# Optimization experiments

Measured on AMD Instinct MI355X. Metric: run time of the kernel, lower is better.

Reference implementation:

```python
import jax, jax.numpy as jnp
import numpy as np

N, D = 8192, 1024

def setup_inputs() -> dict:
    key = jax.random.key(0)
    ks = jax.random.split(key, 7)
    s = 1.0 / np.sqrt(D)
    return {
        "sent_mat": jax.random.normal(ks[0], (N, D), dtype=jnp.float32),
        "indicator": 0,
        "Wq": jax.random.normal(ks[1], (D, D), dtype=jnp.float32) * s,
        "bq": jax.random.normal(ks[2], (D,), dtype=jnp.float32) * s,
        "Wk": jax.random.normal(ks[3], (D, D), dtype=jnp.float32) * s,
        "bk": jax.random.normal(ks[4], (D,), dtype=jnp.float32) * s,
        "Wv": jax.random.normal(ks[5], (D, D), dtype=jnp.float32) * s,
        "bv": jax.random.normal(ks[6], (D,), dtype=jnp.float32) * s,
    }

def reference(sent_mat, indicator, Wq, bq, Wk, bk, Wv, bv):
    # torch.nn.Linear: y = x @ W.T + b
    Q = sent_mat @ Wq.T + bq            # [N, D]
    K = sent_mat @ Wk.T + bk            # [N, D]
    V = sent_mat @ Wv.T + bv            # [N, D]
    sim = Q @ K.T                       # [N, N]
    if indicator == 0:                  # custom score inversion
        sim = 1.0 - sim
    sim_norm = sim / jnp.sqrt(jnp.asarray(D, dtype=sim.dtype))
    # NOTE: softmax over dim=0 (columns normalized over rows), unconventional
    attn_w = jax.nn.softmax(sim_norm, axis=0)   # [N, N]
    attn_out = attn_w @ V               # [N, D]
    return (attn_out, attn_w)
```

## Files before the change

kernel.cpp:

```cpp
#include <hip/hip_runtime.h>

#define NT 8192
#define DM 1024

typedef unsigned short u16;
typedef __bf16 bf16x8 __attribute__((ext_vector_type(8)));
typedef float f32x4 __attribute__((ext_vector_type(4)));
typedef u16 u16x8 __attribute__((ext_vector_type(8)));

__device__ __forceinline__ u16 f2bf(float f) {
  union { float f; unsigned u; } v; v.f = f;
  unsigned r = v.u + 0x7fffu + ((v.u >> 16) & 1u);
  return (u16)(r >> 16);
}
__device__ __forceinline__ float bf2f(u16 h) {
  union { unsigned u; float f; } v; v.u = ((unsigned)h) << 16;
  return v.f;
}

__device__ __forceinline__ void stage16(const u16* g, u16* lds_wave_uniform) {
  __builtin_amdgcn_global_load_lds(
      (const __attribute__((address_space(1))) unsigned int*)g,
      (__attribute__((address_space(3))) unsigned int*)lds_wave_uniform, 16, 0, 0);
}

__global__ void cvt_bf16_kernel(const float* __restrict__ in, u16* __restrict__ out, int n4) {
  int i = blockIdx.x * blockDim.x + threadIdx.x;
  int stride = gridDim.x * blockDim.x;
  for (; i < n4; i += stride) {
    float4 v = reinterpret_cast<const float4*>(in)[i];
    ushort4 o;
    o.x = f2bf(v.x); o.y = f2bf(v.y); o.z = f2bf(v.z); o.w = f2bf(v.w);
    reinterpret_cast<ushort4*>(out)[i] = o;
  }
}

__global__ __launch_bounds__(512, 2)
void qkt_exp_256(const u16* __restrict__ Q, const u16* __restrict__ Kmat, int K,
                 u16* __restrict__ E, float* __restrict__ cs,
                 const int* __restrict__ indp) {
  __shared__ u16 AT[2][256 * 64];
  __shared__ u16 BT[2][256 * 64];
  const int t = threadIdx.x;
  const int l = t & 63;
  const int w = t >> 6;
  const int wm = w >> 2;
  const int wn = w & 3;
  const int r16 = l & 15;
  const int half = l >> 4;

  const int gx = gridDim.x;
  const int nwg = gx * gridDim.y;
  int lin = blockIdx.y * gx + blockIdx.x;
  if ((nwg & 7) == 0) lin = (lin & 7) * (nwg >> 3) + (lin >> 3);
  const int bx = lin % gx;
  const int by = lin / gx;
  const size_t brow = (size_t)by * 256;
  const size_t bcol = (size_t)bx * 256;

  const int srow = w * 8 + (l >> 3);
  const int kel = ((l & 7) ^ (l >> 3)) * 8;
  const int ntiles = K >> 6;

  f32x4 acc[8][4] = {};

#pragma unroll
  for (int q = 0; q < 4; ++q) {
    stage16(Q    + (brow + q * 64 + srow) * (size_t)K + kel, &AT[0][q * 4096 + w * 512]);
    stage16(Kmat + (bcol + q * 64 + srow) * (size_t)K + kel, &BT[0][q * 4096 + w * 512]);
  }
  __syncthreads();

  for (int tt = 0; tt < ntiles; ++tt) {
    const int cur = tt & 1;
    const int nxt = cur ^ 1;
    const int k1 = (tt + 1) << 6;
    const bool more = (tt + 1 < ntiles);
#pragma unroll
    for (int p = 0; p < 4; ++p) {
      if (p == 0 && more) {
#pragma unroll
        for (int q = 0; q < 4; ++q)
          stage16(Q + (brow + q * 64 + srow) * (size_t)K + (k1 + kel),
                  &AT[nxt][q * 4096 + w * 512]);
      }
      if (p == 1 && more) {
#pragma unroll
        for (int q = 0; q < 4; ++q)
          stage16(Kmat + (bcol + q * 64 + srow) * (size_t)K + (k1 + kel),
                  &BT[nxt][q * 4096 + w * 512]);
      }
      bf16x8 af[4][2], bfr[2][2];
#pragma unroll
      for (int m = 0; m < 4; ++m) {
        const int row = wm * 128 + (p >> 1) * 64 + m * 16 + r16;
#pragma unroll
        for (int kk = 0; kk < 2; ++kk) {
          const int slot = (half + 4 * kk) ^ (r16 & 7);
          af[m][kk] = *reinterpret_cast<const bf16x8*>(&AT[cur][row * 64 + slot * 8]);
        }
      }
#pragma unroll
      for (int n = 0; n < 2; ++n) {
        const int row = wn * 64 + (p & 1) * 32 + n * 16 + r16;
#pragma unroll
        for (int kk = 0; kk < 2; ++kk) {
          const int slot = (half + 4 * kk) ^ (r16 & 7);
          bfr[n][kk] = *reinterpret_cast<const bf16x8*>(&BT[cur][row * 64 + slot * 8]);
        }
      }
      __builtin_amdgcn_s_setprio(1);
#pragma unroll
      for (int m = 0; m < 4; ++m)
#pragma unroll
        for (int n = 0; n < 2; ++n)
#pragma unroll
          for (int kk = 0; kk < 2; ++kk)
            acc[(p >> 1) * 4 + m][(p & 1) * 2 + n] = __builtin_amdgcn_mfma_f32_16x16x32_bf16(
                af[m][kk], bfr[n][kk], acc[(p >> 1) * 4 + m][(p & 1) * 2 + n], 0, 0, 0);
      __builtin_amdgcn_s_setprio(0);
      __builtin_amdgcn_sched_barrier(0);
    }
    __syncthreads();
  }

  const bool flip = (*indp == 0);
  const float cexp = 0.045084220027780106f;
  float csum[4] = {0.f, 0.f, 0.f, 0.f};
#pragma unroll
  for (int mg = 0; mg < 8; ++mg) {
#pragma unroll
    for (int ng = 0; ng < 4; ++ng) {
#pragma unroll
      for (int q = 0; q < 4; ++q) {
        float s = acc[mg][ng][q];
        float x = flip ? (1.0f - s) : s;
        float e = exp2f(x * cexp);
        size_t row = brow + wm * 128 + mg * 16 + half * 4 + q;
        size_t col = bcol + wn * 64 + ng * 16 + r16;
        E[row * NT + col] = f2bf(e);
        csum[ng] += e;
      }
    }
  }
#pragma unroll
  for (int ng = 0; ng < 4; ++ng) {
    float s = csum[ng];
    s += __shfl_xor(s, 16);
    s += __shfl_xor(s, 32);
    if (l < 16) atomicAdd(&cs[bcol + wn * 64 + ng * 16 + l], s);
  }
}

template<int EPI>
__global__ __launch_bounds__(512, 2)
void mega_bt(const u16* __restrict__ A, const u16* __restrict__ B, int K, int ldo,
             const float* __restrict__ bias, u16* __restrict__ obf,
             float* __restrict__ of32, float* __restrict__ cs,
             const int* __restrict__ indp) {
  __shared__ u16 AT[3][256 * 64];
  __shared__ u16 BT[3][128 * 64];
  const int t = threadIdx.x;
  const int l = t & 63;
  const int w = t >> 6;
  const int wm = w >> 2;
  const int wn = w & 3;
  const int r16 = l & 15;
  const int half = l >> 4;

  const int gx = gridDim.x;
  const int nwg = gx * gridDim.y;
  int lin = blockIdx.y * gx + blockIdx.x;
  if ((nwg & 7) == 0) lin = (lin & 7) * (nwg >> 3) + (lin >> 3);
  const int bx = lin % gx;
  const int by = lin / gx;
  const size_t brow = (size_t)by * 256;
  const size_t bcol = (size_t)bx * 128;

  const int srow = w * 8 + (l >> 3);
  const int kel = ((l & 7) ^ (l >> 3)) * 8;
  const int nt = K >> 6;

  f32x4 acc[8][2] = {};

#define STAGE(tile, buf)                                                              \
  {                                                                                   \
    const int k0_ = (tile) << 6;                                                      \
    _Pragma("unroll")                                                                 \
    for (int q = 0; q < 4; ++q)                                                       \
      stage16(A + (brow + q * 64 + srow) * (size_t)K + (k0_ + kel),                   \
              &AT[buf][q * 4096 + w * 512]);                                          \
    _Pragma("unroll")                                                                 \
    for (int q = 0; q < 2; ++q)                                                       \
      stage16(B + (bcol + q * 64 + srow) * (size_t)K + (k0_ + kel),                   \
              &BT[buf][q * 4096 + w * 512]);                                          \
  }

  STAGE(0, 0);
  STAGE(1, 1);

  for (int tt = 0; tt < nt; ++tt) {
    const int cur = tt % 3;
    if (tt < nt - 1) asm volatile("s_waitcnt vmcnt(6)" ::: "memory");
    else             asm volatile("s_waitcnt vmcnt(0)" ::: "memory");
    __builtin_amdgcn_s_barrier();
    __builtin_amdgcn_sched_barrier(0);
    if (tt + 2 < nt) STAGE(tt + 2, (tt + 2) % 3);
    __builtin_amdgcn_sched_barrier(0);

    bf16x8 bfr[2][2];
#pragma unroll
    for (int n = 0; n < 2; ++n) {
      const int row = wn * 32 + n * 16 + r16;
#pragma unroll
      for (int kk = 0; kk < 2; ++kk) {
        const int slot = (half + 4 * kk) ^ (r16 & 7);
        bfr[n][kk] = *reinterpret_cast<const bf16x8*>(&BT[cur][row * 64 + slot * 8]);
      }
    }
#pragma unroll
    for (int p = 0; p < 2; ++p) {
      bf16x8 af[4][2];
#pragma unroll
      for (int m = 0; m < 4; ++m) {
        const int row = wm * 128 + p * 64 + m * 16 + r16;
#pragma unroll
        for (int kk = 0; kk < 2; ++kk) {
          const int slot = (half + 4 * kk) ^ (r16 & 7);
          af[m][kk] = *reinterpret_cast<const bf16x8*>(&AT[cur][row * 64 + slot * 8]);
        }
      }
      __builtin_amdgcn_s_setprio(1);
#pragma unroll
      for (int m = 0; m < 4; ++m)
#pragma unroll
        for (int n = 0; n < 2; ++n)
#pragma unroll
          for (int kk = 0; kk < 2; ++kk)
            acc[p * 4 + m][n] = __builtin_amdgcn_mfma_f32_16x16x32_bf16(
                af[m][kk], bfr[n][kk], acc[p * 4 + m][n], 0, 0, 0);
      __builtin_amdgcn_s_setprio(0);
      __builtin_amdgcn_sched_barrier(0);
    }
  }
#undef STAGE

  if constexpr (EPI == 0) {
#pragma unroll
    for (int mg = 0; mg < 8; ++mg) {
#pragma unroll
      for (int n = 0; n < 2; ++n) {
        const int cc = wn * 32 + n * 16 + r16;
        const float bv = bias[bcol + cc];
#pragma unroll
        for (int q = 0; q < 4; ++q) {
          size_t row = brow + wm * 128 + mg * 16 + half * 4 + q;
          obf[row * (size_t)ldo + bcol + cc] = f2bf(acc[mg][n][q] + bv);
        }
      }
    }
  } else if constexpr (EPI == 1) {
    const bool flip = (*indp == 0);
    const float cexp = 0.045084220027780106f;
    float csum[2] = {0.f, 0.f};
#pragma unroll
    for (int mg = 0; mg < 8; ++mg) {
#pragma unroll
      for (int n = 0; n < 2; ++n) {
        const int cc = wn * 32 + n * 16 + r16;
#pragma unroll
        for (int q = 0; q < 4; ++q) {
          float s = acc[mg][n][q];
          float x = flip ? (1.0f - s) : s;
          float e = exp2f(x * cexp);
          size_t row = brow + wm * 128 + mg * 16 + half * 4 + q;
          obf[row * (size_t)ldo + bcol + cc] = f2bf(e);
          csum[n] += e;
        }
      }
    }
#pragma unroll
    for (int n = 0; n < 2; ++n) {
      float s = csum[n];
      s += __shfl_xor(s, 16);
      s += __shfl_xor(s, 32);
      if (l < 16) atomicAdd(&cs[bcol + wn * 32 + n * 16 + l], s);
    }
  } else {
#pragma unroll
    for (int mg = 0; mg < 8; ++mg) {
#pragma unroll
      for (int n = 0; n < 2; ++n) {
#pragma unroll
        for (int q = 0; q < 4; ++q) {
          size_t row = brow + wm * 128 + mg * 16 + half * 4 + q;
          size_t col = bcol + wn * 32 + n * 16 + r16;
          of32[row * (size_t)ldo + col] = acc[mg][n][q];
        }
      }
    }
  }
}

template<int EPI, int AF32, int BF32>
__global__ __launch_bounds__(256)
void gemm_bt(const void* __restrict__ Av, const void* __restrict__ Bv, int K, int ldo,
             const float* __restrict__ bias, u16* __restrict__ obf,
             float* __restrict__ of32, const int* __restrict__ indp) {
  __shared__ u16 As[128 * 32];
  __shared__ u16 Bs[128 * 32];
  const int t = threadIdx.x;
  const int l = t & 63;
  const int w = t >> 6;
  const int wr = w >> 1;
  const int wc = w & 1;
  const int r16 = l & 15;
  const int half = l >> 4;

  const int gx = gridDim.x;
  const int nwg = gx * gridDim.y;
  int lin = blockIdx.y * gx + blockIdx.x;
  if ((nwg & 7) == 0) lin = (lin & 7) * (nwg >> 3) + (lin >> 3);
  const int bx = lin % gx;
  const int by = lin / gx;

  const size_t brow = (size_t)by * 128;
  const size_t bcol = (size_t)bx * 128;
  const int kel = (l & 3) * 8;
  const int lrow = l >> 2;

  f32x4 acc[4][4] = {};

  for (int k0 = 0; k0 < K; k0 += 32) {
#pragma unroll
    for (int c = 0; c < 2; ++c) {
      const int seg = c * 4 + w;
      const int r = seg * 16 + lrow;
      if constexpr (AF32) {
        const float* ga = (const float*)Av + (brow + r) * (size_t)K + (k0 + kel);
        float4 u0 = *reinterpret_cast<const float4*>(ga);
        float4 u1 = *reinterpret_cast<const float4*>(ga + 4);
        u16x8 o;
        o[0] = f2bf(u0.x); o[1] = f2bf(u0.y); o[2] = f2bf(u0.z); o[3] = f2bf(u0.w);
        o[4] = f2bf(u1.x); o[5] = f2bf(u1.y); o[6] = f2bf(u1.z); o[7] = f2bf(u1.w);
        *reinterpret_cast<u16x8*>(&As[seg * 512 + l * 8]) = o;
      } else {
        const u16* ga = (const u16*)Av + (brow + r) * (size_t)K + (k0 + kel);
        stage16(ga, &As[seg * 512]);
      }
      if constexpr (BF32) {
        const float* gb = (const float*)Bv + (bcol + r) * (size_t)K + (k0 + kel);
        float4 u0 = *reinterpret_cast<const float4*>(gb);
        float4 u1 = *reinterpret_cast<const float4*>(gb + 4);
        u16x8 o;
        o[0] = f2bf(u0.x); o[1] = f2bf(u0.y); o[2] = f2bf(u0.z); o[3] = f2bf(u0.w);
        o[4] = f2bf(u1.x); o[5] = f2bf(u1.y); o[6] = f2bf(u1.z); o[7] = f2bf(u1.w);
        *reinterpret_cast<u16x8*>(&Bs[seg * 512 + l * 8]) = o;
      } else {
        const u16* gb = (const u16*)Bv + (bcol + r) * (size_t)K + (k0 + kel);
        stage16(gb, &Bs[seg * 512]);
      }
    }
    __syncthreads();
    bf16x8 af[4], bfv[4];
#pragma unroll
    for (int m = 0; m < 4; ++m)
      af[m] = *reinterpret_cast<const bf16x8*>(&As[(wr * 64 + m * 16 + r16) * 32 + half * 8]);
#pragma unroll
    for (int n = 0; n < 4; ++n)
      bfv[n] = *reinterpret_cast<const bf16x8*>(&Bs[(wc * 64 + n * 16 + r16) * 32 + half * 8]);
#pragma unroll
    for (int m = 0; m < 4; ++m)
#pragma unroll
      for (int n = 0; n < 4; ++n)
        acc[m][n] = __builtin_amdgcn_mfma_f32_16x16x32_bf16(af[m], bfv[n], acc[m][n], 0, 0, 0);
    __syncthreads();
  }

  const int crow0 = wr * 64 + half * 4;
  const int ccol0 = wc * 64 + r16;

  if constexpr (EPI == 0) {
#pragma unroll
    for (int m = 0; m < 4; ++m) {
#pragma unroll
      for (int n = 0; n < 4; ++n) {
        const int cc = ccol0 + n * 16;
        const float bv = bias[bcol + cc];
#pragma unroll
        for (int q = 0; q < 4; ++q) {
          size_t idx = (brow + crow0 + m * 16 + q) * (size_t)ldo + (bcol + cc);
          obf[idx] = f2bf(acc[m][n][q] + bv);
        }
      }
    }
  } else if constexpr (EPI == 1) {
    const bool flip = (*indp == 0);
    const float cexp = 0.045084220027780106f;
#pragma unroll
    for (int m = 0; m < 4; ++m) {
#pragma unroll
      for (int n = 0; n < 4; ++n) {
        const int cc = ccol0 + n * 16;
#pragma unroll
        for (int q = 0; q < 4; ++q) {
          float s = acc[m][n][q];
          float x = flip ? (1.0f - s) : s;
          size_t idx = (brow + crow0 + m * 16 + q) * (size_t)ldo + (bcol + cc);
          of32[idx] = exp2f(x * cexp);
        }
      }
    }
  } else {
#pragma unroll
    for (int m = 0; m < 4; ++m) {
#pragma unroll
      for (int n = 0; n < 4; ++n) {
        const int cc = ccol0 + n * 16;
#pragma unroll
        for (int q = 0; q < 4; ++q) {
          size_t idx = (brow + crow0 + m * 16 + q) * (size_t)ldo + (bcol + cc);
          of32[idx] = acc[m][n][q];
        }
      }
    }
  }
}

__global__ void colsum_kernel(const float* __restrict__ E, float* __restrict__ cs) {
  const int col = blockIdx.x * 256 + threadIdx.x;
  const int r0 = blockIdx.y * 256;
  float s = 0.f;
  for (int r = r0; r < r0 + 256; ++r)
    s += E[(size_t)r * NT + col];
  atomicAdd(&cs[col], s);
}

__global__ void norm_kernel(float* __restrict__ w, const float* __restrict__ cs, int n4) {
  int i = blockIdx.x * blockDim.x + threadIdx.x;
  int stride = gridDim.x * blockDim.x;
  for (; i < n4; i += stride) {
    float4 v = reinterpret_cast<float4*>(w)[i];
    int j4 = i & (NT / 4 - 1);
    float4 c = reinterpret_cast<const float4*>(cs)[j4];
    v.x /= c.x; v.y /= c.y; v.z /= c.z; v.w /= c.w;
    reinterpret_cast<float4*>(w)[i] = v;
  }
}

__global__ void norm_bf16_kernel(const u16* __restrict__ e, float* __restrict__ w,
                                 const float* __restrict__ cs, int n4) {
  int i = blockIdx.x * blockDim.x + threadIdx.x;
  int stride = gridDim.x * blockDim.x;
  for (; i < n4; i += stride) {
    ushort4 ev = reinterpret_cast<const ushort4*>(e)[i];
    int j4 = i & (NT / 4 - 1);
    float4 c = reinterpret_cast<const float4*>(cs)[j4];
    float4 v;
    v.x = bf2f(ev.x) / c.x;
    v.y = bf2f(ev.y) / c.y;
    v.z = bf2f(ev.z) / c.z;
    v.w = bf2f(ev.w) / c.w;
    reinterpret_cast<float4*>(w)[i] = v;
  }
}

__global__ void vt_kernel(const u16* __restrict__ Vb, const float* __restrict__ cs,
                          u16* __restrict__ Vt) {
  __shared__ u16 tile[64][65];
  const int jb = blockIdx.x * 64;
  const int db = blockIdx.y * 64;
  const int t = threadIdx.x;
  {
    const int d = t & 63;
    const int j0 = t >> 6;
    for (int jj = j0; jj < 64; jj += 4)
      tile[jj][d] = Vb[(size_t)(jb + jj) * DM + db + d];
  }
  __syncthreads();
  {
    const int j = t & 63;
    const int d0 = t >> 6;
    const float inv = cs ? (1.0f / cs[jb + j]) : 1.0f;
    for (int dd = d0; dd < 64; dd += 4) {
      u16 raw = tile[j][dd];
      Vt[(size_t)(db + dd) * NT + jb + j] = cs ? f2bf(bf2f(raw) * inv) : raw;
    }
  }
}

extern "C" void kernel_launch(void* const* d_in, const int* in_sizes, int n_in,
                              void* d_out, int out_size, void* d_ws, size_t ws_size,
                              hipStream_t stream) {
  const float* X  = (const float*)d_in[0];
  const int* indp = (const int*)d_in[1];
  const float* Wq = (const float*)d_in[2];
  const float* bq = (const float*)d_in[3];
  const float* Wk = (const float*)d_in[4];
  const float* bk = (const float*)d_in[5];
  const float* Wv = (const float*)d_in[6];
  const float* bv = (const float*)d_in[7];

  float* attn_out = (float*)d_out;
  float* attn_w   = (float*)d_out + (size_t)NT * DM;

  const size_t EB_BYTES = (size_t)NT * NT * 2;
  const size_t QKV_BYTES = (size_t)NT * DM * 2;
  const size_t need_fast = EB_BYTES + 4 * QKV_BYTES + NT * 4;

  if (ws_size >= need_fast) {
    char* ws = (char*)d_ws;
    u16* Eb = (u16*)ws;
    u16* Qb = (u16*)(ws + EB_BYTES);
    u16* Kb = Qb + (size_t)NT * DM;
    u16* Vb = Kb + (size_t)NT * DM;
    u16* Vt = Vb + (size_t)NT * DM;
    float* cs = (float*)(Vt + (size_t)NT * DM);
    u16* Xb  = Eb;
    u16* Wqb = Eb + (size_t)NT * DM;
    u16* Wkb = Wqb + (size_t)DM * DM;
    u16* Wvb = Wkb + (size_t)DM * DM;

    cvt_bf16_kernel<<<2048, 256, 0, stream>>>(X,  Xb,  NT * DM / 4);
    cvt_bf16_kernel<<<1024, 256, 0, stream>>>(Wq, Wqb, DM * DM / 4);
    cvt_bf16_kernel<<<1024, 256, 0, stream>>>(Wk, Wkb, DM * DM / 4);
    cvt_bf16_kernel<<<1024, 256, 0, stream>>>(Wv, Wvb, DM * DM / 4);

    dim3 gqkv(DM / 128, NT / 256);
    mega_bt<0><<<gqkv, 512, 0, stream>>>(Xb, Wqb, DM, DM, bq, Qb, nullptr, nullptr, nullptr);
    mega_bt<0><<<gqkv, 512, 0, stream>>>(Xb, Wkb, DM, DM, bk, Kb, nullptr, nullptr, nullptr);
    mega_bt<0><<<gqkv, 512, 0, stream>>>(Xb, Wvb, DM, DM, bv, Vb, nullptr, nullptr, nullptr);

    hipMemsetAsync(cs, 0, NT * sizeof(float), stream);
    qkt_exp_256<<<dim3(NT / 256, NT / 256), 512, 0, stream>>>(Qb, Kb, DM, Eb, cs, indp);

    vt_kernel<<<dim3(NT / 64, DM / 64), 256, 0, stream>>>(Vb, cs, Vt);

    mega_bt<2><<<dim3(DM / 128, NT / 256), 512, 0, stream>>>(
        Eb, Vt, NT, DM, nullptr, nullptr, attn_out, nullptr, nullptr);

    norm_bf16_kernel<<<4096, 256, 0, stream>>>(Eb, attn_w, cs, NT * NT / 4);
  } else {
    char* ws = (char*)d_ws;
    u16* Qb = (u16*)ws;  ws += QKV_BYTES;
    u16* Kb = (u16*)ws;  ws += QKV_BYTES;
    u16* Vb = (u16*)ws;  ws += QKV_BYTES;
    u16* Vt = (u16*)ws;  ws += QKV_BYTES;
    float* cs = (float*)ws;

    dim3 gqkv(DM / 128, NT / 128);
    gemm_bt<0, 1, 1><<<gqkv, 256, 0, stream>>>(X, Wq, DM, DM, bq, Qb, nullptr, nullptr);
    gemm_bt<0, 1, 1><<<gqkv, 256, 0, stream>>>(X, Wk, DM, DM, bk, Kb, nullptr, nullptr);
    gemm_bt<0, 1, 1><<<gqkv, 256, 0, stream>>>(X, Wv, DM, DM, bv, Vb, nullptr, nullptr);

    gemm_bt<1, 0, 0><<<dim3(NT / 128, NT / 128), 256, 0, stream>>>(
        Qb, Kb, DM, NT, nullptr, nullptr, attn_w, indp);

    hipMemsetAsync(cs, 0, NT * sizeof(float), stream);
    colsum_kernel<<<dim3(32, 32), 256, 0, stream>>>(attn_w, cs);
    norm_kernel<<<4096, 256, 0, stream>>>(attn_w, cs, NT * NT / 4);
    vt_kernel<<<dim3(NT / 64, DM / 64), 256, 0, stream>>>(Vb, nullptr, Vt);

    gemm_bt<2, 1, 0><<<dim3(DM / 128, NT / 128), 256, 0, stream>>>(
        attn_w, Vt, NT, DM, nullptr, nullptr, attn_out, nullptr);
  }
}
```

Measured before the change: 512.6 us.

## Fuse attention-weight normalization into the E@V GEMM and merge bf16 conversions

The separate pass that reads the bf16 exp matrix and writes normalized fp32 attention weights is removed. The E@V GEMM now writes those weights itself from the A tiles already staged in LDS, with each column-block workgroup covering its own slice of K columns. This drops one full read of the 8192x8192 bf16 matrix, at the cost of heavy fp32 global stores inside the GEMM main loop that may stall its pipeline. The four fp32-to-bf16 conversion launches are also merged into one kernel to cut launch overhead.

After: 514.8 us. About the same (+0.4%).

```diff
diff --git a/kernel.cpp b/kernel.cpp
--- a/kernel.cpp
+++ b/kernel.cpp
@@ -24,14 +24,25 @@
       (__attribute__((address_space(3))) unsigned int*)lds_wave_uniform, 16, 0, 0);
 }
 
-__global__ void cvt_bf16_kernel(const float* __restrict__ in, u16* __restrict__ out, int n4) {
+__global__ void cvt_all_kernel(const float* __restrict__ X, const float* __restrict__ Wq,
+                               const float* __restrict__ Wk, const float* __restrict__ Wv,
+                               u16* __restrict__ Xb, u16* __restrict__ Wqb,
+                               u16* __restrict__ Wkb, u16* __restrict__ Wvb) {
+  const int NX = NT * DM / 4;
+  const int NW = DM * DM / 4;
+  const int total = NX + 3 * NW;
   int i = blockIdx.x * blockDim.x + threadIdx.x;
   int stride = gridDim.x * blockDim.x;
-  for (; i < n4; i += stride) {
-    float4 v = reinterpret_cast<const float4*>(in)[i];
+  for (; i < total; i += stride) {
+    const float* src; u16* dst; int j;
+    if (i < NX)               { src = X;  dst = Xb;  j = i; }
+    else if (i < NX + NW)     { src = Wq; dst = Wqb; j = i - NX; }
+    else if (i < NX + 2 * NW) { src = Wk; dst = Wkb; j = i - NX - NW; }
+    else                      { src = Wv; dst = Wvb; j = i - NX - 2 * NW; }
+    float4 v = reinterpret_cast<const float4*>(src)[j];
     ushort4 o;
     o.x = f2bf(v.x); o.y = f2bf(v.y); o.z = f2bf(v.z); o.w = f2bf(v.w);
-    reinterpret_cast<ushort4*>(out)[i] = o;
+    reinterpret_cast<ushort4*>(dst)[j] = o;
   }
 }
 
@@ -157,7 +168,7 @@
 void mega_bt(const u16* __restrict__ A, const u16* __restrict__ B, int K, int ldo,
              const float* __restrict__ bias, u16* __restrict__ obf,
              float* __restrict__ of32, float* __restrict__ cs,
-             const int* __restrict__ indp) {
+             float* __restrict__ wf32, const int* __restrict__ indp) {
   __shared__ u16 AT[3][256 * 64];
   __shared__ u16 BT[3][128 * 64];
   const int t = threadIdx.x;
@@ -242,6 +253,20 @@
       __builtin_amdgcn_s_setprio(0);
       __builtin_amdgcn_sched_barrier(0);
     }
+
+    if constexpr (EPI == 3) {
+      if ((tt >> 4) == bx) {
+        const int kg = (tt << 6) + l;
+        const float invc = 1.0f / cs[kg];
+#pragma unroll
+        for (int wi = 0; wi < 32; ++wi) {
+          const int row = w * 32 + wi;
+          const int slot = (l >> 3) ^ (row & 7);
+          u16 ev = AT[cur][row * 64 + slot * 8 + (l & 7)];
+          wf32[(brow + row) * (size_t)NT + kg] = bf2f(ev) * invc;
+        }
+      }
+    }
   }
 #undef STAGE
 
@@ -258,33 +283,6 @@
           obf[row * (size_t)ldo + bcol + cc] = f2bf(acc[mg][n][q] + bv);
         }
       }
-    }
-  } else if constexpr (EPI == 1) {
-    const bool flip = (*indp == 0);
-    const float cexp = 0.045084220027780106f;
-    float csum[2] = {0.f, 0.f};
-#pragma unroll
-    for (int mg = 0; mg < 8; ++mg) {
-#pragma unroll
-      for (int n = 0; n < 2; ++n) {
-        const int cc = wn * 32 + n * 16 + r16;
-#pragma unroll
-        for (int q = 0; q < 4; ++q) {
-          float s = acc[mg][n][q];
-          float x = flip ? (1.0f - s) : s;
-          float e = exp2f(x * cexp);
-          size_t row = brow + wm * 128 + mg * 16 + half * 4 + q;
-          obf[row * (size_t)ldo + bcol + cc] = f2bf(e);
-          csum[n] += e;
-        }
-      }
-    }
-#pragma unroll
-    for (int n = 0; n < 2; ++n) {
-      float s = csum[n];
-      s += __shfl_xor(s, 16);
-      s += __shfl_xor(s, 32);
-      if (l < 16) atomicAdd(&cs[bcol + wn * 32 + n * 16 + l], s);
     }
   } else {
 #pragma unroll
@@ -448,23 +446,6 @@
   }
 }
 
-__global__ void norm_bf16_kernel(const u16* __restrict__ e, float* __restrict__ w,
-                                 const float* __restrict__ cs, int n4) {
-  int i = blockIdx.x * blockDim.x + threadIdx.x;
-  int stride = gridDim.x * blockDim.x;
-  for (; i < n4; i += stride) {
-    ushort4 ev = reinterpret_cast<const ushort4*>(e)[i];
-    int j4 = i & (NT / 4 - 1);
-    float4 c = reinterpret_cast<const float4*>(cs)[j4];
-    float4 v;
-    v.x = bf2f(ev.x) / c.x;
-    v.y = bf2f(ev.y) / c.y;
-    v.z = bf2f(ev.z) / c.z;
-    v.w = bf2f(ev.w) / c.w;
-    reinterpret_cast<float4*>(w)[i] = v;
-  }
-}
-
 __global__ void vt_kernel(const u16* __restrict__ Vb, const float* __restrict__ cs,
                           u16* __restrict__ Vt) {
   __shared__ u16 tile[64][65];
@@ -521,25 +502,20 @@
     u16* Wkb = Wqb + (size_t)DM * DM;
     u16* Wvb = Wkb + (size_t)DM * DM;
 
-    cvt_bf16_kernel<<<2048, 256, 0, stream>>>(X,  Xb,  NT * DM / 4);
-    cvt_bf16_kernel<<<1024, 256, 0, stream>>>(Wq, Wqb, DM * DM / 4);
-    cvt_bf16_kernel<<<1024, 256, 0, stream>>>(Wk, Wkb, DM * DM / 4);
-    cvt_bf16_kernel<<<1024, 256, 0, stream>>>(Wv, Wvb, DM * DM / 4);
+    cvt_all_kernel<<<2048, 256, 0, stream>>>(X, Wq, Wk, Wv, Xb, Wqb, Wkb, Wvb);
 
     dim3 gqkv(DM / 128, NT / 256);
-    mega_bt<0><<<gqkv, 512, 0, stream>>>(Xb, Wqb, DM, DM, bq, Qb, nullptr, nullptr, nullptr);
-    mega_bt<0><<<gqkv, 512, 0, stream>>>(Xb, Wkb, DM, DM, bk, Kb, nullptr, nullptr, nullptr);
-    mega_bt<0><<<gqkv, 512, 0, stream>>>(Xb, Wvb, DM, DM, bv, Vb, nullptr, nullptr, nullptr);
+    mega_bt<0><<<gqkv, 512, 0, stream>>>(Xb, Wqb, DM, DM, bq, Qb, nullptr, nullptr, nullptr, nullptr);
+    mega_bt<0><<<gqkv, 512, 0, stream>>>(Xb, Wkb, DM, DM, bk, Kb, nullptr, nullptr, nullptr, nullptr);
+    mega_bt<0><<<gqkv, 512, 0, stream>>>(Xb, Wvb, DM, DM, bv, Vb, nullptr, nullptr, nullptr, nullptr);
 
     hipMemsetAsync(cs, 0, NT * sizeof(float), stream);
     qkt_exp_256<<<dim3(NT / 256, NT / 256), 512, 0, stream>>>(Qb, Kb, DM, Eb, cs, indp);
 
     vt_kernel<<<dim3(NT / 64, DM / 64), 256, 0, stream>>>(Vb, cs, Vt);
 
-    mega_bt<2><<<dim3(DM / 128, NT / 256), 512, 0, stream>>>(
-        Eb, Vt, NT, DM, nullptr, nullptr, attn_out, nullptr, nullptr);
-
-    norm_bf16_kernel<<<4096, 256, 0, stream>>>(Eb, attn_w, cs, NT * NT / 4);
+    mega_bt<3><<<dim3(DM / 128, NT / 256), 512, 0, stream>>>(
+        Eb, Vt, NT, DM, nullptr, nullptr, attn_out, cs, attn_w, nullptr);
   } else {
     char* ws = (char*)d_ws;
     u16* Qb = (u16*)ws;  ws += QKV_BYTES;
```
